# Performance work log

Hardware: AMD Instinct MI355X
Metric: run time of the kernel (lower is better)

## Reference

```python
import jax, jax.numpy as jnp
import numpy as np

B, S, E = 2, 1024, 1024
H, DH = 16, 64           # num_heads, key_dim = E // H
MAXLEN = 2048            # config.max_sequence_length -> table size 2*MAXLEN-1


def setup_inputs() -> dict:
    key = jax.random.key(0)
    ks = jax.random.split(key, 13)
    sc = 1.0 / np.sqrt(E)
    return {
        "query": jax.random.normal(ks[0], (B, S, E), jnp.float32),
        "key": jax.random.normal(ks[1], (B, S, E), jnp.float32),
        "value": jax.random.normal(ks[2], (B, S, E), jnp.float32),
        "Wq": jax.random.normal(ks[3], (E, E), jnp.float32) * sc,
        "bq": jnp.zeros((E,), jnp.float32),
        "Wk": jax.random.normal(ks[4], (E, E), jnp.float32) * sc,
        "bk": jnp.zeros((E,), jnp.float32),
        "Wv": jax.random.normal(ks[5], (E, E), jnp.float32) * sc,
        "bv": jnp.zeros((E,), jnp.float32),
        "Wo": jax.random.normal(ks[6], (E, E), jnp.float32) * sc,
        "bo": jnp.zeros((E,), jnp.float32),
        "rel_pos_emb": jax.random.normal(ks[7], (2 * MAXLEN - 1, DH), jnp.float32) * 0.02,
        "rel_pos_bias": jnp.zeros((2 * MAXLEN - 1,), jnp.float32),
    }


def _split_heads(x):
    # [B, S, E] -> [B, H, S, DH]
    return x.reshape(B, S, H, DH).transpose(0, 2, 1, 3)


def _relative_shift(x):
    # x: [B, H, S, S]; pad one zero column on the left of the last dim,
    # reshape to [B, H, S+1, S], drop the first row -> [B, H, S, S]
    x = jnp.pad(x, ((0, 0), (0, 0), (0, 0), (1, 0)))
    x = x.reshape(B, H, S + 1, S)
    return x[:, :, 1:, :]


def reference(query, key, value, Wq, bq, Wk, bk, Wv, bv, Wo, bo,
              rel_pos_emb, rel_pos_bias):
    q = _split_heads(query @ Wq + bq) / jnp.sqrt(jnp.float32(DH))  # [B,H,S,DH]
    k = _split_heads(key @ Wk + bk)                                 # [B,H,S,DH]
    v = _split_heads(value @ Wv + bv)                               # [B,H,S,DH]

    scores = jnp.einsum("bhid,bhjd->bhij", q, k)  # [B,H,S,S]

    # relative position term (gather + skew, as in the original call())
    pos_ids = jnp.arange(S)[:, None] - jnp.arange(S)[None, :] + (MAXLEN - 1)  # [S,S]
    rpe = rel_pos_emb[pos_ids]    # [S, S, DH]
    rpb = rel_pos_bias[pos_ids]   # [S, S]
    rel = jnp.einsum("bhid,ijd->bhij", q, rpe)  # [B,H,S,S]
    rel = _relative_shift(rel)
    scores = scores + rel + rpb   # rpb broadcasts over [B,H]

    weights = jax.nn.softmax(scores, axis=-1)
    out = jnp.einsum("bhij,bhjd->bhid", weights, v)  # [B,H,S,DH]
    out = out.transpose(0, 2, 1, 3).reshape(B, S, E)
    return out @ Wo + bo
```

## Files before the change

### kernel.cpp

```cpp
#include <hip/hip_runtime.h>

typedef unsigned short u16;
typedef __bf16 bf16_t;
typedef bf16_t bf16x8 __attribute__((ext_vector_type(8)));
typedef u16 u16x8 __attribute__((ext_vector_type(8)));
typedef float f32x4 __attribute__((ext_vector_type(4)));

#define DEVI __device__ __forceinline__


DEVI u16 f2bf(float f) {
    unsigned u = __builtin_bit_cast(unsigned, f);
    u = (u + 0x7FFFu + ((u >> 16) & 1u)) >> 16;
    return (u16)u;
}
DEVI float bf2f(u16 b) {
    unsigned u = ((unsigned)b) << 16;
    return __builtin_bit_cast(float, u);
}
DEVI f32x4 mfma16(u16x8 a, u16x8 b, f32x4 c) {
    return __builtin_amdgcn_mfma_f32_16x16x32_bf16(
        __builtin_bit_cast(bf16x8, a), __builtin_bit_cast(bf16x8, b), c, 0, 0, 0);
}
DEVI void gl2lds(const u16* g, u16* l) {
    __builtin_amdgcn_global_load_lds(
        (__attribute__((address_space(1))) void*)g,
        (__attribute__((address_space(3))) void*)l, 16, 0, 0);
}

__global__ __launch_bounds__(256) void cvt_kernel(
    const float* __restrict__ q, const float* __restrict__ k, const float* __restrict__ v,
    const float* __restrict__ emb,
    u16* __restrict__ xq, u16* __restrict__ xk, u16* __restrict__ xv, u16* __restrict__ embb)
{
    const long NQ = 2097152;
    const long NE = 262080;
    long i4 = ((long)blockIdx.x * 256 + threadIdx.x) * 4;
    if (i4 < 3 * NQ) {
        int which = (int)(i4 >> 21);
        long off = i4 & (NQ - 1);
        const float* src = which == 0 ? q : (which == 1 ? k : v);
        u16* dst = which == 0 ? xq : (which == 1 ? xk : xv);
        float4 f = *(const float4*)(src + off);
        ushort4 o; o.x = f2bf(f.x); o.y = f2bf(f.y); o.z = f2bf(f.z); o.w = f2bf(f.w);
        *(ushort4*)(dst + off) = o;
    } else {
        long off = i4 - 3 * NQ;
        if (off < NE) {
            float4 f = *(const float4*)(emb + off);
            ushort4 o; o.x = f2bf(f.x); o.y = f2bf(f.y); o.z = f2bf(f.z); o.w = f2bf(f.w);
            *(ushort4*)(embb + off) = o;
        }
    }
}

__global__ __launch_bounds__(256) void wt_kernel(
    const float* __restrict__ w0, const float* __restrict__ w1,
    const float* __restrict__ w2, const float* __restrict__ w3,
    u16* __restrict__ t0, u16* __restrict__ t1, u16* __restrict__ t2, u16* __restrict__ t3)
{
    int z = blockIdx.z;
    const float* W = z == 0 ? w0 : (z == 1 ? w1 : (z == 2 ? w2 : w3));
    u16* T = z == 0 ? t0 : (z == 1 ? t1 : (z == 2 ? t2 : t3));
    __shared__ float tile[64][65];
    int k0 = blockIdx.y * 64, n0 = blockIdx.x * 64;
    int tx = threadIdx.x, ty = threadIdx.y;
    for (int r = ty; r < 64; r += 4)
        tile[r][tx] = W[(long)(k0 + r) * 1024 + n0 + tx];
    __syncthreads();
    for (int r = ty; r < 64; r += 4)
        T[(long)(n0 + r) * 1024 + k0 + tx] = f2bf(tile[tx][r]);
}

template<int MT>
__global__ __launch_bounds__(256) void gemm_kernel(
    const u16* __restrict__ A0, const u16* __restrict__ A1, const u16* __restrict__ A2,
    const u16* __restrict__ W0, const u16* __restrict__ W1, const u16* __restrict__ W2,
    const float* __restrict__ bias0, const float* __restrict__ bias1, const float* __restrict__ bias2,
    u16* __restrict__ o0, u16* __restrict__ o1, u16* __restrict__ o2,
    float* __restrict__ ofp, int mode_base)
{
    int z = blockIdx.z;
    int mode = mode_base + z;
    const u16* A = z == 0 ? A0 : (z == 1 ? A1 : A2);
    const u16* W = z == 0 ? W0 : (z == 1 ? W1 : W2);
    const float* bias = z == 0 ? bias0 : (z == 1 ? bias1 : bias2);
    u16* ob = z == 0 ? o0 : (z == 1 ? o1 : o2);

    constexpr int MROWS = MT * 32;
    __shared__ u16 la[2 * MROWS * 32];
    __shared__ u16 lw[2 * 128 * 32];

    int lin = blockIdx.x + (blockIdx.y << 3);
    int xcd = lin & 7, idx = lin >> 3;
    int xt = (xcd & 1) * 4 + (idx & 3);
    int yt = (xcd >> 1) * 8 + (idx >> 2);
    int m0 = yt * MROWS, n0 = xt * 128;

    int t = threadIdx.x, lane = t & 63, wid = t >> 6;
    int l15 = lane & 15, quad = lane >> 4;
    int wm = (wid >> 1) * (MT * 16), wn = (wid & 1) * 64;
    int sr = lane >> 2, sp = lane & 3;

    f32x4 acc[MT][4] = {};

    auto stage = [&](int buf, int k0) {
#pragma unroll
        for (int q = 0; q < MT / 2; q++) {
            int r = wid * (MT * 8) + q * 16 + sr;
            int c = sp ^ ((r >> 1) & 3);
            gl2lds(A + (long)(m0 + r) * 1024 + k0 + c * 8,
                   la + buf * (MROWS * 32) + (wid * (MT * 8) + q * 16) * 32);
        }
#pragma unroll
        for (int q = 0; q < 2; q++) {
            int r = wid * 32 + q * 16 + sr;
            int c = sp ^ ((r >> 1) & 3);
            gl2lds(W + (long)(n0 + r) * 1024 + k0 + c * 8,
                   lw + buf * (128 * 32) + (wid * 32 + q * 16) * 32);
        }
    };

    stage(0, 0);
    __syncthreads();
    int cur = 0;
#pragma unroll 1
    for (int k0 = 0; k0 < 1024; k0 += 32) {
        if (k0 < 992) stage(cur ^ 1, k0 + 32);
        const u16* lab = la + cur * (MROWS * 32);
        const u16* lwb = lw + cur * (128 * 32);
        u16x8 af[MT], bfr[4];
#pragma unroll
        for (int mt = 0; mt < MT; mt++) {
            int r = wm + mt * 16 + l15;
            af[mt] = *(const u16x8*)&lab[r * 32 + ((quad ^ ((r >> 1) & 3)) * 8)];
        }
#pragma unroll
        for (int nt = 0; nt < 4; nt++) {
            int r = wn + nt * 16 + l15;
            bfr[nt] = *(const u16x8*)&lwb[r * 32 + ((quad ^ ((r >> 1) & 3)) * 8)];
        }
#pragma unroll
        for (int mt = 0; mt < MT; mt++)
#pragma unroll
            for (int nt = 0; nt < 4; nt++)
                acc[mt][nt] = mfma16(af[mt], bfr[nt], acc[mt][nt]);
        __syncthreads();
        cur ^= 1;
    }

#pragma unroll
    for (int mt = 0; mt < MT; mt++)
#pragma unroll
        for (int nt = 0; nt < 4; nt++)
#pragma unroll
            for (int reg = 0; reg < 4; reg++) {
                int gm = m0 + wm + mt * 16 + quad * 4 + reg;
                int gn = n0 + wn + nt * 16 + l15;
                float val = acc[mt][nt][reg] + bias[gn];
                if (mode == 0) {
                    val *= 0.125f;
                    long o = ((long)((gm >> 10) * 16 + (gn >> 6)) << 16) + ((gm & 1023) << 6) + (gn & 63);
                    ob[o] = f2bf(val);
                } else if (mode == 1) {
                    long o = ((long)((gm >> 10) * 16 + (gn >> 6)) << 16) + ((gm & 1023) << 6) + (gn & 63);
                    ob[o] = f2bf(val);
                } else if (mode == 2) {
                    long o = ((long)((gm >> 10) * 16 + (gn >> 6)) << 16) + ((long)(gn & 63) << 10) + (gm & 1023);
                    ob[o] = f2bf(val);
                } else {
                    ofp[(long)gm * 1024 + gn] = val;
                }
            }
}

__global__ __launch_bounds__(256) void gc_kernel(
    const u16* __restrict__ qb, const u16* __restrict__ embb,
    const float* __restrict__ rpb, u16* __restrict__ Bskew)
{
    int u0 = blockIdx.x * 32;
    int i0 = u0 & 1023;
    int t = threadIdx.x, lane = t & 63, wid = t >> 6;
    int l15 = lane & 15, quad = lane >> 4;

    __shared__ float lds_rpb[2048];
    for (int j = t; j < 1024; j += 256) {
        lds_rpb[j] = rpb[j + 2047];
        lds_rpb[1024 + j] = rpb[j + 1022];
    }
    __syncthreads();

    u16x8 aq[2][2];
#pragma unroll
    for (int rg = 0; rg < 2; rg++) {
        long qoff = (long)(u0 + rg * 16 + l15) * 64 + quad * 8;
        aq[rg][0] = *(const u16x8*)&qb[qoff];
        aq[rg][1] = *(const u16x8*)&qb[qoff + 32];
    }

    u16x8 nb0, nb1;
    {
        long ebase = (long)(1024 + i0 + wid * 16 + l15) * 64 + quad * 8;
        nb0 = *(const u16x8*)&embb[ebase];
        nb1 = *(const u16x8*)&embb[ebase + 32];
    }

    for (int tt = wid; tt < 66; tt += 4) {
        u16x8 b0 = nb0, b1 = nb1;
        if (tt + 4 < 66) {
            long ebase = (long)(1024 + i0 + (tt + 4) * 16 + l15) * 64 + quad * 8;
            nb0 = *(const u16x8*)&embb[ebase];
            nb1 = *(const u16x8*)&embb[ebase + 32];
        }
        int w0 = tt * 16;
#pragma unroll
        for (int rg = 0; rg < 2; rg++) {
            f32x4 c = {};
            c = mfma16(aq[rg][0], b0, c);
            c = mfma16(aq[rg][1], b1, c);
#pragma unroll
            for (int reg = 0; reg < 4; reg++) {
                int row = rg * 16 + quad * 4 + reg;
                int cc = w0 + l15 - row;
                if ((unsigned)cc <= 1023u) {
                    int i = i0 + row;
                    float rb = lds_rpb[cc + ((cc <= i) ? 0 : 1024)];
                    Bskew[((long)(u0 + row) << 10) + cc] = f2bf(c[reg] + rb);
                }
            }
        }
    }
}

__global__ __launch_bounds__(256, 3) void flash_kernel(
    const u16* __restrict__ qb, const u16* __restrict__ kb, const u16* __restrict__ vT,
    const u16* __restrict__ Bskew, const float* __restrict__ rpb,
    float* __restrict__ Po, float* __restrict__ Pm, float* __restrict__ Pl)
{
    int itile = blockIdx.x;
    int bh = blockIdx.y;
    int js = blockIdx.z;
    int t = threadIdx.x, lane = t & 63, wid = t >> 6;
    int l15 = lane & 15, quad = lane >> 4;
    int i0w = itile * 64 + wid * 16;

    __shared__ u16 lds_k[2][64 * 64];
    __shared__ u16 lds_v[2][64 * 64];
    __shared__ u16 lds_p[4][16][72];

    int sr8 = lane >> 3, sp8 = lane & 7;

    float rpb2046 = rpb[2046];

    u16x8 aq[2];
    {
        long qoff = ((long)(bh * 1024) + i0w + l15) * 64 + quad * 8;
        aq[0] = *(const u16x8*)&qb[qoff];
        aq[1] = *(const u16x8*)&qb[qoff + 32];
    }
    float m_r[4], l_r[4];
    f32x4 o_acc[4] = {};
#pragma unroll
    for (int r = 0; r < 4; r++) { m_r[r] = -1e30f; l_r[r] = 0.f; }

    const u16* kbase = kb + (long)bh * 65536;
    const u16* vbase = vT + (long)bh * 65536;
    const u16* bbase = Bskew + ((long)bh << 20);

    auto stage = [&](int buf, int j0) {
#pragma unroll
        for (int q = 0; q < 2; q++) {
            int r = wid * 16 + q * 8 + sr8;
            int c = sp8 ^ (r & 7);
            gl2lds(kbase + (long)(j0 + r) * 64 + c * 8, &lds_k[buf][(wid * 16 + q * 8) * 64]);
            gl2lds(vbase + (long)r * 1024 + j0 + c * 8, &lds_v[buf][(wid * 16 + q * 8) * 64]);
        }
    };
    auto ldb = [&](int j0, unsigned short* b) {
#pragma unroll
        for (int nt = 0; nt < 4; nt++) {
            int jn0 = j0 + nt * 16;
            int jj = jn0 + l15;
            if (jn0 + 15 <= i0w) {
#pragma unroll
                for (int reg = 0; reg < 4; reg++) {
                    int ii = i0w + quad * 4 + reg;
                    b[nt * 4 + reg] = bbase[((long)ii << 10) + (ii - jj)];
                }
            } else if (jn0 >= i0w + 17) {
#pragma unroll
                for (int reg = 0; reg < 4; reg++) {
                    int ii = i0w + quad * 4 + reg;
                    b[nt * 4 + reg] = bbase[((long)(ii + 1) << 10) + (ii + 1025 - jj)];
                }
            } else {
#pragma unroll
                for (int reg = 0; reg < 4; reg++) {
                    int ii = i0w + quad * 4 + reg;
                    long off = (jj <= ii) ? (((long)ii << 10) + (ii - jj))
                             : ((jj == ii + 1) ? ((long)ii << 10)
                                               : (((long)(ii + 1) << 10) + (ii + 1025 - jj)));
                    b[nt * 4 + reg] = bbase[off];
                }
            }
        }
    };

    unsigned short bcur[16], bnxt[16];
    stage(0, js * 512);
    ldb(js * 512, bcur);
    __syncthreads();

    int cur = 0;
    for (int jt = 0; jt < 8; jt++) {
        int j0 = js * 512 + jt * 64;
        if (jt < 7) {
            stage(cur ^ 1, j0 + 64);
            ldb(j0 + 64, bnxt);
        }

        f32x4 s_acc[4];
#pragma unroll
        for (int nt = 0; nt < 4; nt++) {
            int r = nt * 16 + l15;
            u16x8 b0 = *(const u16x8*)&lds_k[cur][r * 64 + ((quad ^ (r & 7)) * 8)];
            u16x8 b1 = *(const u16x8*)&lds_k[cur][r * 64 + (((quad + 4) ^ (r & 7)) * 8)];
            f32x4 c = {};
            c = mfma16(aq[0], b0, c);
            c = mfma16(aq[1], b1, c);
            s_acc[nt] = c;
        }

#pragma unroll
        for (int nt = 0; nt < 4; nt++) {
            int jn0 = j0 + nt * 16;
            int jj = jn0 + l15;
            bool mixed = (jn0 + 15 > i0w) && (jn0 < i0w + 17);
#pragma unroll
            for (int reg = 0; reg < 4; reg++) {
                int ii = i0w + quad * 4 + reg;
                float a = bf2f(bcur[nt * 4 + reg]);
                if (mixed && jj == ii + 1) a = rpb2046;
                s_acc[nt][reg] += a;
            }
        }

#pragma unroll
        for (int reg = 0; reg < 4; reg++) {
            float mx = fmaxf(fmaxf(s_acc[0][reg], s_acc[1][reg]), fmaxf(s_acc[2][reg], s_acc[3][reg]));
            for (int off = 1; off < 16; off <<= 1) mx = fmaxf(mx, __shfl_xor(mx, off, 64));
            float mnew = fmaxf(m_r[reg], mx);
            float alpha = __expf(m_r[reg] - mnew);
            float rs = 0.f;
#pragma unroll
            for (int nt = 0; nt < 4; nt++) {
                float p = __expf(s_acc[nt][reg] - mnew);
                s_acc[nt][reg] = p;
                rs += p;
            }
            for (int off = 1; off < 16; off <<= 1) rs += __shfl_xor(rs, off, 64);
            l_r[reg] = l_r[reg] * alpha + rs;
            m_r[reg] = mnew;
#pragma unroll
            for (int dt = 0; dt < 4; dt++) o_acc[dt][reg] *= alpha;
        }

#pragma unroll
        for (int nt = 0; nt < 4; nt++)
#pragma unroll
            for (int reg = 0; reg < 4; reg++)
                lds_p[wid][quad * 4 + reg][nt * 16 + l15] = f2bf(s_acc[nt][reg]);

        u16x8 pf0 = *(const u16x8*)&lds_p[wid][l15][quad * 8];
        u16x8 pf1 = *(const u16x8*)&lds_p[wid][l15][quad * 8 + 32];
#pragma unroll
        for (int dt = 0; dt < 4; dt++) {
            int r = dt * 16 + l15;
            u16x8 v0 = *(const u16x8*)&lds_v[cur][r * 64 + ((quad ^ (r & 7)) * 8)];
            u16x8 v1 = *(const u16x8*)&lds_v[cur][r * 64 + (((quad + 4) ^ (r & 7)) * 8)];
            o_acc[dt] = mfma16(pf0, v0, o_acc[dt]);
            o_acc[dt] = mfma16(pf1, v1, o_acc[dt]);
        }

        __syncthreads();
        cur ^= 1;
        if (jt < 7) {
#pragma unroll
            for (int q = 0; q < 16; q++) bcur[q] = bnxt[q];
        }
    }

    int blk = (js * 32 + bh) * 16 + itile;
    float* PoB = Po + (long)blk * 4096;
#pragma unroll
    for (int dt = 0; dt < 4; dt++)
#pragma unroll
        for (int reg = 0; reg < 4; reg++) {
            int rr = wid * 16 + quad * 4 + reg;
            PoB[rr * 64 + dt * 16 + l15] = o_acc[dt][reg];
        }
    if (l15 == 0) {
#pragma unroll
        for (int reg = 0; reg < 4; reg++) {
            int rr = wid * 16 + quad * 4 + reg;
            Pm[blk * 64 + rr] = m_r[reg];
            Pl[blk * 64 + rr] = l_r[reg];
        }
    }
}

__global__ __launch_bounds__(256) void combine_kernel(
    const float* __restrict__ Po, const float* __restrict__ Pm, const float* __restrict__ Pl,
    u16* __restrict__ attn)
{
    int itile = blockIdx.x, bh = blockIdx.y;
    int t = threadIdx.x;
    int c = t & 63, rg = t >> 6;
    int blk0 = bh * 16 + itile;
    int blk1 = (32 + bh) * 16 + itile;
    int b = bh >> 4, h = bh & 15;
    for (int rr = rg; rr < 64; rr += 4) {
        float m0 = Pm[blk0 * 64 + rr], m1 = Pm[blk1 * 64 + rr];
        float ms = fmaxf(m0, m1);
        float e0 = __expf(m0 - ms), e1 = __expf(m1 - ms);
        float l = Pl[blk0 * 64 + rr] * e0 + Pl[blk1 * 64 + rr] * e1;
        float o = Po[(long)blk0 * 4096 + rr * 64 + c] * e0
                + Po[(long)blk1 * 4096 + rr * 64 + c] * e1;
        int ii = itile * 64 + rr;
        attn[((long)(b * 1024 + ii)) * 1024 + h * 64 + c] = f2bf(o / l);
    }
}

extern "C" void kernel_launch(void* const* d_in, const int* in_sizes, int n_in,
                              void* d_out, int out_size, void* d_ws, size_t ws_size,
                              hipStream_t stream)
{
    const float* query = (const float*)d_in[0];
    const float* key_  = (const float*)d_in[1];
    const float* value = (const float*)d_in[2];
    const float* Wq = (const float*)d_in[3];
    const float* bq = (const float*)d_in[4];
    const float* Wk = (const float*)d_in[5];
    const float* bk = (const float*)d_in[6];
    const float* Wv = (const float*)d_in[7];
    const float* bv = (const float*)d_in[8];
    const float* Wo = (const float*)d_in[9];
    const float* bo = (const float*)d_in[10];
    const float* emb = (const float*)d_in[11];
    const float* rpb = (const float*)d_in[12];

    char* ws = (char*)d_ws;
    u16* xq   = (u16*)(ws + 0);
    u16* xk   = (u16*)(ws + 4194304);
    u16* xv   = (u16*)(ws + 8388608);
    u16* WqT  = (u16*)(ws + 12582912);
    u16* WkT  = (u16*)(ws + 14680064);
    u16* WvT  = (u16*)(ws + 16777216);
    u16* embb = (u16*)(ws + 18874368);
    u16* WoT  = (u16*)(ws + 19922944);
    u16* qb   = (u16*)(ws + 22020096);
    u16* kb   = (u16*)(ws + 26214400);
    u16* vT   = (u16*)(ws + 30408704);
    u16* Bskew= (u16*)(ws + 34603008);
    float* Po = (float*)(ws + 0);
    float* Pm = (float*)(ws + 16777216);
    float* Pl = (float*)(ws + 17039360);
    u16* attn = (u16*)(ws + 22020096);

    cvt_kernel<<<6400, 256, 0, stream>>>(query, key_, value, emb, xq, xk, xv, embb);
    wt_kernel<<<dim3(16, 16, 4), dim3(64, 4), 0, stream>>>(Wq, Wk, Wv, Wo, WqT, WkT, WvT, WoT);
    gemm_kernel<2><<<dim3(8, 32, 3), 256, 0, stream>>>(xq, xk, xv, WqT, WkT, WvT,
                                                       bq, bk, bv, qb, kb, vT, nullptr, 0);
    gc_kernel<<<1024, 256, 0, stream>>>(qb, embb, rpb, Bskew);
    flash_kernel<<<dim3(16, 32, 2), 256, 0, stream>>>(qb, kb, vT, Bskew, rpb, Po, Pm, Pl);
    combine_kernel<<<dim3(16, 32), 256, 0, stream>>>(Po, Pm, Pl, attn);
    gemm_kernel<2><<<dim3(8, 32, 1), 256, 0, stream>>>(attn, nullptr, nullptr, WoT, nullptr, nullptr,
                                                       bo, nullptr, nullptr,
                                                       nullptr, nullptr, nullptr, (float*)d_out, 3);
}
```

Baseline: 263.5 us.

## Replace double-buffered LDS K/V staging with register prefetch and single buffer

K/V tiles were staged through direct global-to-LDS copies into two buffers. They are now prefetched into registers one tile ahead and written into a single LDS buffer at the top of each iteration, with a barrier after the write. This halves the K/V LDS footprint, and the launch bound is raised from 3 to 4 blocks per CU to gain occupancy. The cost is more VGPRs for the prefetched tiles, an extra register-to-LDS write per iteration, and a register budget that may now cause spills.

```diff
diff --git a/kernel.cpp b/kernel.cpp
--- a/kernel.cpp
+++ b/kernel.cpp
@@ -232,7 +232,7 @@
     }
 }
 
-__global__ __launch_bounds__(256, 3) void flash_kernel(
+__global__ __launch_bounds__(256, 4) void flash_kernel(
     const u16* __restrict__ qb, const u16* __restrict__ kb, const u16* __restrict__ vT,
     const u16* __restrict__ Bskew, const float* __restrict__ rpb,
     float* __restrict__ Po, float* __restrict__ Pm, float* __restrict__ Pl)
@@ -244,11 +244,13 @@
     int l15 = lane & 15, quad = lane >> 4;
     int i0w = itile * 64 + wid * 16;
 
-    __shared__ u16 lds_k[2][64 * 64];
-    __shared__ u16 lds_v[2][64 * 64];
+    __shared__ u16 lds_k[64 * 64];
+    __shared__ u16 lds_v[64 * 64];
     __shared__ u16 lds_p[4][16][72];
 
     int sr8 = lane >> 3, sp8 = lane & 7;
+    int rS0 = wid * 16 + sr8,     cS0 = sp8 ^ (rS0 & 7);
+    int rS1 = wid * 16 + 8 + sr8, cS1 = sp8 ^ (rS1 & 7);
 
     float rpb2046 = rpb[2046];
 
@@ -267,16 +269,19 @@
     const u16* vbase = vT + (long)bh * 65536;
     const u16* bbase = Bskew + ((long)bh << 20);
 
-    auto stage = [&](int buf, int j0) {
-#pragma unroll
-        for (int q = 0; q < 2; q++) {
-            int r = wid * 16 + q * 8 + sr8;
-            int c = sp8 ^ (r & 7);
-            gl2lds(kbase + (long)(j0 + r) * 64 + c * 8, &lds_k[buf][(wid * 16 + q * 8) * 64]);
-            gl2lds(vbase + (long)r * 1024 + j0 + c * 8, &lds_v[buf][(wid * 16 + q * 8) * 64]);
-        }
+    auto ldKV = [&](int j0, u16x8* kr, u16x8* vr) {
+        kr[0] = *(const u16x8*)(kbase + (long)(j0 + rS0) * 64 + cS0 * 8);
+        kr[1] = *(const u16x8*)(kbase + (long)(j0 + rS1) * 64 + cS1 * 8);
+        vr[0] = *(const u16x8*)(vbase + (long)rS0 * 1024 + j0 + cS0 * 8);
+        vr[1] = *(const u16x8*)(vbase + (long)rS1 * 1024 + j0 + cS1 * 8);
     };
-    auto ldb = [&](int j0, unsigned short* b) {
+    auto wrKV = [&](const u16x8* kr, const u16x8* vr) {
+        *(u16x8*)&lds_k[(wid * 16) * 64 + lane * 8] = kr[0];
+        *(u16x8*)&lds_k[(wid * 16 + 8) * 64 + lane * 8] = kr[1];
+        *(u16x8*)&lds_v[(wid * 16) * 64 + lane * 8] = vr[0];
+        *(u16x8*)&lds_v[(wid * 16 + 8) * 64 + lane * 8] = vr[1];
+    };
+    auto ldb = [&](int j0, unsigned short (&b)[16]) {
 #pragma unroll
         for (int nt = 0; nt < 4; nt++) {
             int jn0 = j0 + nt * 16;
@@ -306,16 +311,18 @@
         }
     };
 
+    u16x8 krC[2], vrC[2], krN[2], vrN[2];
     unsigned short bcur[16], bnxt[16];
-    stage(0, js * 512);
+    ldKV(js * 512, krC, vrC);
     ldb(js * 512, bcur);
-    __syncthreads();
-
-    int cur = 0;
+
     for (int jt = 0; jt < 8; jt++) {
         int j0 = js * 512 + jt * 64;
+        wrKV(krC, vrC);
+        __syncthreads();
+
         if (jt < 7) {
-            stage(cur ^ 1, j0 + 64);
+            ldKV(j0 + 64, krN, vrN);
             ldb(j0 + 64, bnxt);
         }
 
@@ -323,8 +330,8 @@
 #pragma unroll
         for (int nt = 0; nt < 4; nt++) {
             int r = nt * 16 + l15;
-            u16x8 b0 = *(const u16x8*)&lds_k[cur][r * 64 + ((quad ^ (r & 7)) * 8)];
-            u16x8 b1 = *(const u16x8*)&lds_k[cur][r * 64 + (((quad + 4) ^ (r & 7)) * 8)];
+            u16x8 b0 = *(const u16x8*)&lds_k[r * 64 + ((quad ^ (r & 7)) * 8)];
+            u16x8 b1 = *(const u16x8*)&lds_k[r * 64 + (((quad + 4) ^ (r & 7)) * 8)];
             f32x4 c = {};
             c = mfma16(aq[0], b0, c);
             c = mfma16(aq[1], b1, c);
@@ -376,15 +383,16 @@
 #pragma unroll
         for (int dt = 0; dt < 4; dt++) {
             int r = dt * 16 + l15;
-            u16x8 v0 = *(const u16x8*)&lds_v[cur][r * 64 + ((quad ^ (r & 7)) * 8)];
-            u16x8 v1 = *(const u16x8*)&lds_v[cur][r * 64 + (((quad + 4) ^ (r & 7)) * 8)];
+            u16x8 v0 = *(const u16x8*)&lds_v[r * 64 + ((quad ^ (r & 7)) * 8)];
+            u16x8 v1 = *(const u16x8*)&lds_v[r * 64 + (((quad + 4) ^ (r & 7)) * 8)];
             o_acc[dt] = mfma16(pf0, v0, o_acc[dt]);
             o_acc[dt] = mfma16(pf1, v1, o_acc[dt]);
         }
 
         __syncthreads();
-        cur ^= 1;
         if (jt < 7) {
+            krC[0] = krN[0]; krC[1] = krN[1];
+            vrC[0] = vrN[0]; vrC[1] = vrN[1];
 #pragma unroll
             for (int q = 0; q < 16; q++) bcur[q] = bnxt[q];
         }
```

Result: slower. 310.8 us (+17.9%).
